# Kernel optimization log

Hardware: AMD Instinct MI355X
Metric: run time of the kernel (lower is better)

The kernel has to match this reference:

```python
import jax, jax.numpy as jnp
import numpy as np

N_WORD, N_TOPIC, N_DOC = 30000, 1000, 15000
D_WORD, D_TOPIC, D_OUT = 300, 300, 128
E = dict(ww=800000, wt=400000, wd=600000, td=300000, tt=150000)
SRC_N = dict(ww=N_WORD, wt=N_WORD, wd=N_WORD, td=N_TOPIC, tt=N_TOPIC)
DST_N = dict(ww=N_WORD, wt=N_TOPIC, wd=N_DOC, td=N_DOC, tt=N_TOPIC)


def setup_inputs() -> dict:
    key = jax.random.key(0)
    ks = iter(jax.random.split(key, 64))
    inp = {}
    inp["feat_word"] = jax.random.normal(next(ks), (N_WORD, D_WORD), jnp.float32)
    inp["feat_topic"] = jax.random.normal(next(ks), (N_TOPIC, D_TOPIC), jnp.float32)
    for et in ["ww", "wt", "wd", "td", "tt"]:
        inp[f"{et}_src"] = jax.random.randint(next(ks), (E[et],), 0, SRC_N[et], jnp.int32)
        inp[f"{et}_dst"] = jax.random.randint(next(ks), (E[et],), 0, DST_N[et], jnp.int32)
        inp[f"{et}_w"] = jax.random.uniform(next(ks), (E[et],), jnp.float32)
        din = D_WORD if et[0] == "w" else D_TOPIC
        inp[f"W_{et}"] = jax.random.normal(next(ks), (din, D_OUT), jnp.float32) / np.float32(np.sqrt(din))
        inp[f"b_{et}"] = jnp.zeros((D_OUT,), jnp.float32)
    return inp


def _mean_agg(Wh, src, dst, w, n_dst):
    # DGL fn.u_mul_e('Wh','weight','m') + fn.mean('m','h'): per-edge message
    # Wh[src] * w, mean-reduced per destination node (0 for isolated nodes).
    m = Wh[src] * w[:, None]                                   # [E, D_OUT]
    s = jax.ops.segment_sum(m, dst, num_segments=n_dst)        # [n_dst, D_OUT]
    c = jax.ops.segment_sum(jnp.ones_like(w), dst, num_segments=n_dst)
    return s / jnp.maximum(c, 1.0)[:, None]


def reference(feat_word, feat_topic,
              ww_src, ww_dst, ww_w, wt_src, wt_dst, wt_w,
              wd_src, wd_dst, wd_w, td_src, td_dst, td_w,
              tt_src, tt_dst, tt_w,
              W_ww, b_ww, W_wt, b_wt, W_wd, b_wd, W_td, b_td, W_tt, b_tt):
    # NOTE: the original forward's causal/noise branch is dead code --
    # `Wh = self.weight[etype](feat_dict[srctype])` overwrites it, so the
    # live math is a plain per-edge-type linear projection of source feats.
    Wh_ww = feat_word @ W_ww + b_ww
    Wh_wt = feat_word @ W_wt + b_wt
    Wh_wd = feat_word @ W_wd + b_wd
    Wh_td = feat_topic @ W_td + b_td
    Wh_tt = feat_topic @ W_tt + b_tt
    # multi_update_all(..., 'sum'): sum the per-etype means per dst node type.
    h_word = _mean_agg(Wh_ww, ww_src, ww_dst, ww_w, N_WORD)
    h_topic = (_mean_agg(Wh_wt, wt_src, wt_dst, wt_w, N_TOPIC)
               + _mean_agg(Wh_tt, tt_src, tt_dst, tt_w, N_TOPIC))
    h_doc = (_mean_agg(Wh_wd, wd_src, wd_dst, wd_w, N_DOC)
             + _mean_agg(Wh_td, td_src, td_dst, td_w, N_DOC))
    return (h_word, h_topic, h_doc)
```

## Files before the change

kernel.cpp:

```cpp
#include <hip/hip_runtime.h>

#define N_WORD 30000
#define N_TOPIC 1000
#define N_DOC 15000
#define DIN 300
#define KP 320
#define DOUT 128

#define E_WW 800000
#define E_WT 400000
#define E_WD 600000
#define E_TD 300000
#define E_TT 150000
#define E_TOTAL 2250000

#define CC_WW 0
#define CC_WT 30000
#define CC_WD 31000
#define CC_TD 46000
#define CC_TT 61000
#define NBINS 62000

#define CAP_WW 80
#define CAP_WT 544
#define CAP_WD 96
#define CAP_TD 56
#define CAP_TT 240
#define SB_WW 0
#define SB_WT (SB_WW + N_WORD * CAP_WW)
#define SB_WD (SB_WT + N_TOPIC * CAP_WT)
#define SB_TD (SB_WD + N_DOC * CAP_WD)
#define SB_TT (SB_TD + N_DOC * CAP_TD)
#define SLOT_TOTAL (SB_TT + N_TOPIC * CAP_TT)

#define NB_WW 59
#define NB_WT 32
#define NB_WD 30
#define NB_TD 30
#define NB_TT 32
#define CB_WW 0
#define CB_WT (CB_WW + 64 * NB_WW)
#define CB_WD (CB_WT + 64 * NB_WT)
#define CB_TD (CB_WD + 96 * NB_WD)
#define CB_TT (CB_TD + 48 * NB_TD)
#define COARSE_TOTAL (CB_TT + 24 * NB_TT)
#define NBK_TOTAL 183

#define CHUNK_BLOCKS 296
#define PREPW_BLOCKS 200

#define GW_BLOCKS 469
#define GT_BLOCKS 16
#define PKP 328

#define GB_TOPIC 250
#define GB_DOC 3750
#define GB_WORD 7500

using half8  = __attribute__((ext_vector_type(8))) _Float16;
using half2v = __attribute__((ext_vector_type(2))) _Float16;
using f32x4  = __attribute__((ext_vector_type(4))) float;

struct SegP {
    const int* src[5];
    const int* dst[5];
    const float* w[5];
};

struct WPtrs {
    const float* W[5];
    const float* b[5];
};

__device__ __forceinline__ void decode_chunk(
    int blk, int& ti, int& hx, int& ch, int& ne, int& nb, int& sh, int& cb)
{
    if (blk < 64)       { ti=0; hx=blk;     ch=12500; ne=E_WW; nb=NB_WW; sh=9; cb=CB_WW; }
    else if (blk < 128) { ti=1; hx=blk-64;  ch=6250;  ne=E_WT; nb=NB_WT; sh=5; cb=CB_WT; }
    else if (blk < 224) { ti=2; hx=blk-128; ch=6250;  ne=E_WD; nb=NB_WD; sh=9; cb=CB_WD; }
    else if (blk < 272) { ti=3; hx=blk-224; ch=6250;  ne=E_TD; nb=NB_TD; sh=9; cb=CB_TD; }
    else                { ti=4; hx=blk-272; ch=6250;  ne=E_TT; nb=NB_TT; sh=5; cb=CB_TT; }
}

__device__ __forceinline__ void decode_bucket(
    int g, int& b, int& nb, int& nblk, int& sh, int& N,
    int& cap, int& sb, int& cc, int& cb, int& bee)
{
    if (g < 59)       { b=g;     nb=NB_WW; nblk=64; sh=9; N=N_WORD;  cap=CAP_WW; sb=SB_WW; cc=CC_WW; cb=CB_WW; bee=800000; }
    else if (g < 91)  { b=g-59;  nb=NB_WT; nblk=64; sh=5; N=N_TOPIC; cap=CAP_WT; sb=SB_WT; cc=CC_WT; cb=CB_WT; bee=1200000; }
    else if (g < 121) { b=g-91;  nb=NB_WD; nblk=96; sh=9; N=N_DOC;   cap=CAP_WD; sb=SB_WD; cc=CC_WD; cb=CB_WD; bee=1800000; }
    else if (g < 151) { b=g-121; nb=NB_TD; nblk=48; sh=9; N=N_DOC;   cap=CAP_TD; sb=SB_TD; cc=CC_TD; cb=CB_TD; bee=2100000; }
    else              { b=g-151; nb=NB_TT; nblk=24; sh=5; N=N_TOPIC; cap=CAP_TT; sb=SB_TT; cc=CC_TT; cb=CB_TT; bee=2250000; }
}

__global__ __launch_bounds__(1024) void count_w(
    SegP S, int* __restrict__ coarse,
    WPtrs WP, _Float16* __restrict__ Wt_word, _Float16* __restrict__ Wt_topic,
    float* __restrict__ bcat_word, float* __restrict__ bcat_topic)
{
    __shared__ int hh[64];
    const int blk = blockIdx.x;
    if (blk < CHUNK_BLOCKS) {
        int ti, hx, ch, ne, nb, sh, cb;
        decode_chunk(blk, ti, hx, ch, ne, nb, sh, cb);
        if (threadIdx.x < 64) hh[threadIdx.x] = 0;
        __syncthreads();
        const int* __restrict__ dst = S.dst[ti];
        int lo = hx * ch;
        int hi = lo + ch; if (hi > ne) hi = ne;
        for (int i = lo + (int)threadIdx.x; i < hi; i += 1024)
            atomicAdd(&hh[dst[i] >> sh], 1);
        __syncthreads();
        if ((int)threadIdx.x < nb)
            coarse[cb + hx * nb + threadIdx.x] = hh[threadIdx.x];
    } else {
        int id = (blk - CHUNK_BLOCKS) * 1024 + (int)threadIdx.x;
        const int total = (384 + 256) * KP;
        if (id >= total) return;
        int ng = id / KP;
        int k = id - ng * KP;
        int mat, n, lng;
        _Float16* Wt;
        float* bc;
        if (ng < 384) { lng = ng; mat = lng >> 7; Wt = Wt_word; bc = bcat_word; }
        else          { lng = ng - 384; mat = 3 + (lng >> 7); Wt = Wt_topic; bc = bcat_topic; }
        n = lng & 127;
        Wt[(size_t)lng * KP + k] =
            (k < DIN) ? (_Float16)WP.W[mat][(size_t)k * DOUT + n] : (_Float16)0.f;
        if (k == 0) bc[lng] = WP.b[mat][n];
    }
}

template <int NJW>
__device__ __forceinline__ void gemm_cs(
    const float* __restrict__ A, int M,
    const _Float16* __restrict__ Wt, const float* __restrict__ bcat,
    _Float16* __restrict__ C, int Cstride, int rowBlk,
    _Float16* __restrict__ ldsA)
{
    const int t = threadIdx.x;
    const int lane = t & 63;
    const int w = t >> 6;
    const int lm = lane & 15;
    const int lq = lane >> 4;
    const int rowBase = rowBlk * 64;
    const int wc = w * (NJW * 16);

#pragma unroll
    for (int i = 0; i < 10; ++i) {
        int id = i * 256 + t;
        int row = id / 40;
        int c8 = id - row * 40;
        int k = c8 * 8;
        int grow = rowBase + row;
        half8 hv = half8{0, 0, 0, 0, 0, 0, 0, 0};
        if (grow < M) {
            const float* ap = A + (size_t)grow * DIN + k;
            if (k + 8 <= DIN) {
                float4 f0 = *(const float4*)ap;
                float4 f1 = *(const float4*)(ap + 4);
                hv = half8{(_Float16)f0.x, (_Float16)f0.y, (_Float16)f0.z,
                           (_Float16)f0.w, (_Float16)f1.x, (_Float16)f1.y,
                           (_Float16)f1.z, (_Float16)f1.w};
            } else if (k < DIN) {
#pragma unroll
                for (int j = 0; j < 8; ++j)
                    if (k + j < DIN) hv[j] = (_Float16)ap[j];
            }
        }
        *(half8*)&ldsA[row * PKP + k] = hv;
    }
    __syncthreads();

    f32x4 acc[4][NJW];
#pragma unroll
    for (int rt = 0; rt < 4; ++rt)
#pragma unroll
        for (int j = 0; j < NJW; ++j) acc[rt][j] = f32x4{0.f, 0.f, 0.f, 0.f};

#pragma unroll
    for (int s = 0; s < 10; ++s) {
        const int k0 = s * 32 + lq * 8;
        half8 bf[NJW];
#pragma unroll
        for (int j = 0; j < NJW; ++j)
            bf[j] = *(const half8*)&Wt[(size_t)(wc + j * 16 + lm) * KP + k0];
        half8 af[4];
#pragma unroll
        for (int rt = 0; rt < 4; ++rt)
            af[rt] = *(const half8*)&ldsA[(rt * 16 + lm) * PKP + k0];
#pragma unroll
        for (int rt = 0; rt < 4; ++rt)
#pragma unroll
            for (int j = 0; j < NJW; ++j)
                acc[rt][j] = __builtin_amdgcn_mfma_f32_16x16x32_f16(
                    af[rt], bf[j], acc[rt][j], 0, 0, 0);
    }

#pragma unroll
    for (int j = 0; j < NJW; ++j) {
        int col = wc + j * 16 + lm;
        float bias = bcat[col];
#pragma unroll
        for (int rt = 0; rt < 4; ++rt) {
#pragma unroll
            for (int reg = 0; reg < 4; ++reg) {
                int gr = rowBase + rt * 16 + lq * 4 + reg;
                if (gr < M)
                    C[(size_t)gr * Cstride + col] =
                        (_Float16)(acc[rt][j][reg] + bias);
            }
        }
    }
}

__global__ __launch_bounds__(256, 3) void pfx_gemm(
    int* __restrict__ coarse,
    const float* __restrict__ featw, const _Float16* __restrict__ Wtw,
    const float* __restrict__ bw, _Float16* __restrict__ Cw,
    const float* __restrict__ featt, const _Float16* __restrict__ Wtt,
    const float* __restrict__ bt, _Float16* __restrict__ Ct)
{
    __shared__ __align__(16) int usmem[10496];
    const int blk = blockIdx.x;
    if (blk == 0) {
        int* ttot = usmem;
        int* tpfx = usmem + 256;
        int g = threadIdx.x;
        int b, nb, nblk, sh, N, cap, sb, cc, cb, bee;
        if (g < NBK_TOTAL) {
            decode_bucket(g, b, nb, nblk, sh, N, cap, sb, cc, cb, bee);
            int tot = 0;
            for (int k = 0; k < nblk; ++k) tot += coarse[cb + k * nb + b];
            ttot[g] = tot;
        }
        __syncthreads();
        if (threadIdx.x == 0) {
            int run = 0;
            for (int i = 0; i < NBK_TOTAL; ++i) { tpfx[i] = run; run += ttot[i]; }
        }
        __syncthreads();
        if (g < NBK_TOTAL) {
            int run = tpfx[g];
            for (int k = 0; k < nblk; ++k) {
                int idx = cb + k * nb + b;
                int v = coarse[idx];
                coarse[idx] = run;
                run += v;
            }
        }
    } else if (blk < 1 + GW_BLOCKS) {
        gemm_cs<6>(featw, N_WORD, Wtw, bw, Cw, 384, blk - 1,
                   (_Float16*)usmem);
    } else {
        gemm_cs<4>(featt, N_TOPIC, Wtt, bt, Ct, 256, blk - 1 - GW_BLOCKS,
                   (_Float16*)usmem);
    }
}

__global__ __launch_bounds__(1024) void pass_a(
    SegP S, const int* __restrict__ coarse, int2* __restrict__ BE)
{
    __shared__ int cur[64];
    int ti, hx, ch, ne, nb, sh, cb;
    decode_chunk(blockIdx.x, ti, hx, ch, ne, nb, sh, cb);
    if ((int)threadIdx.x < nb)
        cur[threadIdx.x] = coarse[cb + hx * nb + threadIdx.x];
    __syncthreads();
    const int* __restrict__ dst = S.dst[ti];
    const int* __restrict__ src = S.src[ti];
    const float* __restrict__ wp = S.w[ti];
    int lo = hx * ch;
    int hi = lo + ch; if (hi > ne) hi = ne;
    for (int i = lo + (int)threadIdx.x; i < hi; i += 1024) {
        int d = dst[i];
        int p = atomicAdd(&cur[d >> sh], 1);
        unsigned short hw = __builtin_bit_cast(unsigned short, (_Float16)wp[i]);
        BE[p] = make_int2(d, src[i] | ((int)hw << 16));
    }
}

__global__ __launch_bounds__(1024) void pass_b(
    const int* __restrict__ coarse, const int2* __restrict__ BE,
    unsigned int* __restrict__ slots, int* __restrict__ cnt)
{
    __shared__ int cl[512];
    int b, nb, nblk, sh, N, cap, sb, cc, cb, bee;
    decode_bucket(blockIdx.x, b, nb, nblk, sh, N, cap, sb, cc, cb, bee);
    const int width = 1 << sh;
    const int n0 = b << sh;
    for (int j = threadIdx.x; j < width; j += 1024) cl[j] = 0;
    __syncthreads();
    int st = coarse[cb + b];
    int en = (b + 1 < nb) ? coarse[cb + b + 1] : bee;
    for (int i = st + (int)threadIdx.x; i < en; i += 1024) {
        int2 q = BE[i];
        int pos = atomicAdd(&cl[q.x - n0], 1);
        if (pos < cap)
            slots[(size_t)sb + (size_t)q.x * cap + pos] = (unsigned int)q.y;
    }
    __syncthreads();
    for (int j = threadIdx.x; j < width; j += 1024) {
        int d = n0 + j;
        if (d < N) cnt[cc + d] = cl[j];
    }
}

#define SV2(v, i) __builtin_shufflevector(v, v, i, i + 1)

__device__ __forceinline__ _Float16 wbits(unsigned int q)
{
    return __builtin_bit_cast(_Float16, (unsigned short)(q >> 16));
}

__device__ __forceinline__ void seg_mean16(
    const unsigned int* __restrict__ slots, int beg, int ce, int c,
    const _Float16* __restrict__ rowbase, int strideh, int ln, int sub,
    float a[8])
{
    half2v ac0 = half2v{0, 0}, ac1 = half2v{0, 0};
    half2v ac2 = half2v{0, 0}, ac3 = half2v{0, 0};
    int e = 0;
    for (; e + 16 <= ce; e += 16) {
        unsigned int q0 = slots[beg + e + 0 + sub];
        unsigned int q1 = slots[beg + e + 4 + sub];
        unsigned int q2 = slots[beg + e + 8 + sub];
        unsigned int q3 = slots[beg + e + 12 + sub];
        half8 v0 = *(const half8*)(rowbase + (size_t)(q0 & 0xFFFFu) * strideh + ln * 8);
        half8 v1 = *(const half8*)(rowbase + (size_t)(q1 & 0xFFFFu) * strideh + ln * 8);
        half8 v2 = *(const half8*)(rowbase + (size_t)(q2 & 0xFFFFu) * strideh + ln * 8);
        half8 v3 = *(const half8*)(rowbase + (size_t)(q3 & 0xFFFFu) * strideh + ln * 8);
        _Float16 h0 = wbits(q0), h1 = wbits(q1), h2 = wbits(q2), h3 = wbits(q3);
        half2v w0 = half2v{h0, h0}, w1 = half2v{h1, h1};
        half2v w2 = half2v{h2, h2}, w3 = half2v{h3, h3};
        ac0 += SV2(v0, 0) * w0 + SV2(v1, 0) * w1 + SV2(v2, 0) * w2 + SV2(v3, 0) * w3;
        ac1 += SV2(v0, 2) * w0 + SV2(v1, 2) * w1 + SV2(v2, 2) * w2 + SV2(v3, 2) * w3;
        ac2 += SV2(v0, 4) * w0 + SV2(v1, 4) * w1 + SV2(v2, 4) * w2 + SV2(v3, 4) * w3;
        ac3 += SV2(v0, 6) * w0 + SV2(v1, 6) * w1 + SV2(v2, 6) * w2 + SV2(v3, 6) * w3;
    }
    for (int e2 = e + sub; e2 < ce; e2 += 4) {
        unsigned int q = slots[beg + e2];
        half8 v = *(const half8*)(rowbase + (size_t)(q & 0xFFFFu) * strideh + ln * 8);
        _Float16 h = wbits(q);
        half2v wp = half2v{h, h};
        ac0 += SV2(v, 0) * wp;
        ac1 += SV2(v, 2) * wp;
        ac2 += SV2(v, 4) * wp;
        ac3 += SV2(v, 6) * wp;
    }
    a[0] = (float)ac0.x; a[1] = (float)ac0.y;
    a[2] = (float)ac1.x; a[3] = (float)ac1.y;
    a[4] = (float)ac2.x; a[5] = (float)ac2.y;
    a[6] = (float)ac3.x; a[7] = (float)ac3.y;
#pragma unroll
    for (int j = 0; j < 8; ++j) {
        a[j] += __shfl_down(a[j], 16);
        a[j] += __shfl_down(a[j], 32);
    }
    float inv = 1.0f / (float)(c > 1 ? c : 1);
#pragma unroll
    for (int j = 0; j < 8; ++j) a[j] *= inv;
}

__global__ __launch_bounds__(256) void gather_all(
    const unsigned int* __restrict__ slots, const int* __restrict__ cnt,
    const _Float16* __restrict__ Wh_word, const _Float16* __restrict__ Wh_topic,
    float* __restrict__ out_word, float* __restrict__ out_topic,
    float* __restrict__ out_doc)
{
    const int b = blockIdx.x;
    const int t = threadIdx.x;
    const int lane = t & 63;
    const int wv = t >> 6;
    const int sub = lane >> 4;
    const int ln = lane & 15;

    float a[8];
    float* outp;
    int node;

    if (b < GB_TOPIC) {
        node = b * 4 + wv;
        int c1 = cnt[CC_WT + node];
        int ce1 = c1 < CAP_WT ? c1 : CAP_WT;
        seg_mean16(slots, SB_WT + node * CAP_WT, ce1, c1, Wh_word + 128, 384, ln, sub, a);
        int c2 = cnt[CC_TT + node];
        int ce2 = c2 < CAP_TT ? c2 : CAP_TT;
        float a2[8];
        seg_mean16(slots, SB_TT + node * CAP_TT, ce2, c2, Wh_topic + 128, 256, ln, sub, a2);
#pragma unroll
        for (int j = 0; j < 8; ++j) a[j] += a2[j];
        outp = out_topic;
    } else if (b < GB_TOPIC + GB_DOC) {
        node = (b - GB_TOPIC) * 4 + wv;
        int c1 = cnt[CC_WD + node];
        int ce1 = c1 < CAP_WD ? c1 : CAP_WD;
        seg_mean16(slots, SB_WD + node * CAP_WD, ce1, c1, Wh_word + 256, 384, ln, sub, a);
        int c2 = cnt[CC_TD + node];
        int ce2 = c2 < CAP_TD ? c2 : CAP_TD;
        float a2[8];
        seg_mean16(slots, SB_TD + node * CAP_TD, ce2, c2, Wh_topic, 256, ln, sub, a2);
#pragma unroll
        for (int j = 0; j < 8; ++j) a[j] += a2[j];
        outp = out_doc;
    } else {
        node = (b - GB_TOPIC - GB_DOC) * 4 + wv;
        int c = cnt[CC_WW + node];
        int ce = c < CAP_WW ? c : CAP_WW;
        seg_mean16(slots, SB_WW + node * CAP_WW, ce, c, Wh_word, 384, ln, sub, a);
        outp = out_word;
    }

    if (sub == 0) {
        float4* o = (float4*)outp + (size_t)node * 32 + ln * 2;
        o[0] = make_float4(a[0], a[1], a[2], a[3]);
        o[1] = make_float4(a[4], a[5], a[6], a[7]);
    }
}

extern "C" void kernel_launch(void* const* d_in, const int* in_sizes, int n_in,
                              void* d_out, int out_size, void* d_ws, size_t ws_size,
                              hipStream_t stream)
{
    const float* feat_word  = (const float*)d_in[0];
    const float* feat_topic = (const float*)d_in[1];

    const int*   ww_src = (const int*)d_in[2];
    const int*   ww_dst = (const int*)d_in[3];
    const float* ww_w   = (const float*)d_in[4];
    const float* W_ww   = (const float*)d_in[5];
    const float* b_ww   = (const float*)d_in[6];

    const int*   wt_src = (const int*)d_in[7];
    const int*   wt_dst = (const int*)d_in[8];
    const float* wt_w   = (const float*)d_in[9];
    const float* W_wt   = (const float*)d_in[10];
    const float* b_wt   = (const float*)d_in[11];

    const int*   wd_src = (const int*)d_in[12];
    const int*   wd_dst = (const int*)d_in[13];
    const float* wd_w   = (const float*)d_in[14];
    const float* W_wd   = (const float*)d_in[15];
    const float* b_wd   = (const float*)d_in[16];

    const int*   td_src = (const int*)d_in[17];
    const int*   td_dst = (const int*)d_in[18];
    const float* td_w   = (const float*)d_in[19];
    const float* W_td   = (const float*)d_in[20];
    const float* b_td   = (const float*)d_in[21];

    const int*   tt_src = (const int*)d_in[22];
    const int*   tt_dst = (const int*)d_in[23];
    const float* tt_w   = (const float*)d_in[24];
    const float* W_tt   = (const float*)d_in[25];
    const float* b_tt   = (const float*)d_in[26];

    char* wsb = (char*)d_ws;
    size_t off = 0;
    _Float16* Wh_word  = (_Float16*)(wsb + off); off += (size_t)N_WORD * 384 * 2;
    _Float16* Wh_topic = (_Float16*)(wsb + off); off += (size_t)N_TOPIC * 256 * 2;
    _Float16* Wt_word  = (_Float16*)(wsb + off); off += (size_t)384 * KP * 2;
    _Float16* Wt_topic = (_Float16*)(wsb + off); off += (size_t)256 * KP * 2;
    float* bcat_word   = (float*)(wsb + off);    off += 384 * 4;
    float* bcat_topic  = (float*)(wsb + off);    off += 256 * 4;
    unsigned int* slots = (unsigned int*)(wsb + off); off += (size_t)SLOT_TOTAL * 4;
    int* cnt_all       = (int*)(wsb + off);      off += (size_t)NBINS * 4;
    int* coarse        = (int*)(wsb + off);      off += (size_t)COARSE_TOTAL * 4;
    int2* BE           = (int2*)(wsb + off);     off += (size_t)E_TOTAL * 8;

    float* out_word  = (float*)d_out;
    float* out_topic = out_word + (size_t)N_WORD * DOUT;
    float* out_doc   = out_topic + (size_t)N_TOPIC * DOUT;

    SegP S;
    S.src[0] = ww_src; S.dst[0] = ww_dst; S.w[0] = ww_w;
    S.src[1] = wt_src; S.dst[1] = wt_dst; S.w[1] = wt_w;
    S.src[2] = wd_src; S.dst[2] = wd_dst; S.w[2] = wd_w;
    S.src[3] = td_src; S.dst[3] = td_dst; S.w[3] = td_w;
    S.src[4] = tt_src; S.dst[4] = tt_dst; S.w[4] = tt_w;

    WPtrs WP;
    WP.W[0] = W_ww; WP.W[1] = W_wt; WP.W[2] = W_wd; WP.W[3] = W_td; WP.W[4] = W_tt;
    WP.b[0] = b_ww; WP.b[1] = b_wt; WP.b[2] = b_wd; WP.b[3] = b_td; WP.b[4] = b_tt;

    count_w<<<CHUNK_BLOCKS + PREPW_BLOCKS, 1024, 0, stream>>>(
        S, coarse, WP, Wt_word, Wt_topic, bcat_word, bcat_topic);
    pfx_gemm<<<1 + GW_BLOCKS + GT_BLOCKS, 256, 0, stream>>>(
        coarse,
        feat_word, Wt_word, bcat_word, Wh_word,
        feat_topic, Wt_topic, bcat_topic, Wh_topic);
    pass_a<<<CHUNK_BLOCKS, 1024, 0, stream>>>(S, coarse, BE);
    pass_b<<<NBK_TOTAL, 1024, 0, stream>>>(coarse, BE, slots, cnt_all);
    gather_all<<<GB_TOPIC + GB_DOC + GB_WORD, 256, 0, stream>>>(
        slots, cnt_all, Wh_word, Wh_topic, out_word, out_topic, out_doc);

    (void)in_sizes; (void)n_in; (void)ws_size;
}
```

Measured before the change: 301.0 us.

## Privatize per-wave LDS histograms, stage GEMM epilogue through LDS, batch prefix loads

The count and scatter passes now keep one LDS histogram per wavefront instead of one per block, which cuts contention on shared-memory atomics. pass_a recounts its chunk so it can give each wave its own offset range. The GEMM epilogue writes results into LDS and then stores coalesced 16-byte rows instead of scattered 2-byte stores. The prefix scan loads counts eight at a time. The costs are an extra read of dst in pass_a and extra barriers in the epilogue, and there is also an odd no-op bias-pointer assignment.

```diff
diff --git a/kernel.cpp b/kernel.cpp
--- a/kernel.cpp
+++ b/kernel.cpp
@@ -98,21 +98,27 @@
     WPtrs WP, _Float16* __restrict__ Wt_word, _Float16* __restrict__ Wt_topic,
     float* __restrict__ bcat_word, float* __restrict__ bcat_topic)
 {
-    __shared__ int hh[64];
+    __shared__ int wcnt[16][64];
     const int blk = blockIdx.x;
     if (blk < CHUNK_BLOCKS) {
         int ti, hx, ch, ne, nb, sh, cb;
         decode_chunk(blk, ti, hx, ch, ne, nb, sh, cb);
-        if (threadIdx.x < 64) hh[threadIdx.x] = 0;
+        const int w = threadIdx.x >> 6;
+        const int lane = threadIdx.x & 63;
+        wcnt[w][lane] = 0;
         __syncthreads();
         const int* __restrict__ dst = S.dst[ti];
         int lo = hx * ch;
         int hi = lo + ch; if (hi > ne) hi = ne;
         for (int i = lo + (int)threadIdx.x; i < hi; i += 1024)
-            atomicAdd(&hh[dst[i] >> sh], 1);
+            atomicAdd(&wcnt[w][dst[i] >> sh], 1);
         __syncthreads();
-        if ((int)threadIdx.x < nb)
-            coarse[cb + hx * nb + threadIdx.x] = hh[threadIdx.x];
+        if ((int)threadIdx.x < nb) {
+            int s = 0;
+#pragma unroll
+            for (int k = 0; k < 16; ++k) s += wcnt[k][threadIdx.x];
+            coarse[cb + hx * nb + threadIdx.x] = s;
+        }
     } else {
         int id = (blk - CHUNK_BLOCKS) * 1024 + (int)threadIdx.x;
         const int total = (384 + 256) * KP;
@@ -197,19 +203,34 @@
                     af[rt], bf[j], acc[rt][j], 0, 0, 0);
     }
 
-#pragma unroll
-    for (int j = 0; j < NJW; ++j) {
-        int col = wc + j * 16 + lm;
-        float bias = bcat[col];
-#pragma unroll
-        for (int rt = 0; rt < 4; ++rt) {
-#pragma unroll
-            for (int reg = 0; reg < 4; ++reg) {
-                int gr = rowBase + rt * 16 + lq * 4 + reg;
-                if (gr < M)
-                    C[(size_t)gr * Cstride + col] =
-                        (_Float16)(acc[rt][j][reg] + bias);
+    const int HCOLS = NJW * 32;
+    const int HPAD = HCOLS + 8;
+    const int nch = HCOLS / 8;
+#pragma unroll
+    for (int h = 0; h < 2; ++h) {
+        __syncthreads();
+        if ((w >> 1) == h) {
+            int wl = w & 1;
+#pragma unroll
+            for (int j = 0; j < NJW; ++j) {
+                int lc = wl * (NJW * 16) + j * 16 + lm;
+                float bias = bcat[h * HCOLS + lc];
+#pragma unroll
+                for (int rt = 0; rt < 4; ++rt)
+#pragma unroll
+                    for (int reg = 0; reg < 4; ++reg)
+                        ldsA[(rt * 16 + lq * 4 + reg) * HPAD + lc] =
+                            (_Float16)(acc[rt][j][reg] + bias);
             }
+        }
+        __syncthreads();
+        for (int id = t; id < 64 * nch; id += 256) {
+            int row = id / nch;
+            int c8 = id - row * nch;
+            int gr = rowBase + row;
+            if (gr < M)
+                *(half8*)&C[(size_t)gr * Cstride + h * HCOLS + c8 * 8] =
+                    *(const half8*)&ldsA[row * HPAD + c8 * 8];
         }
     }
 }
@@ -231,7 +252,13 @@
         if (g < NBK_TOTAL) {
             decode_bucket(g, b, nb, nblk, sh, N, cap, sb, cc, cb, bee);
             int tot = 0;
-            for (int k = 0; k < nblk; ++k) tot += coarse[cb + k * nb + b];
+            for (int k0 = 0; k0 < nblk; k0 += 8) {
+                int v[8];
+#pragma unroll
+                for (int j = 0; j < 8; ++j) v[j] = coarse[cb + (k0 + j) * nb + b];
+#pragma unroll
+                for (int j = 0; j < 8; ++j) tot += v[j];
+            }
             ttot[g] = tot;
         }
         __syncthreads();
@@ -242,11 +269,15 @@
         __syncthreads();
         if (g < NBK_TOTAL) {
             int run = tpfx[g];
-            for (int k = 0; k < nblk; ++k) {
-                int idx = cb + k * nb + b;
-                int v = coarse[idx];
-                coarse[idx] = run;
-                run += v;
+            for (int k0 = 0; k0 < nblk; k0 += 8) {
+                int v[8];
+#pragma unroll
+                for (int j = 0; j < 8; ++j) v[j] = coarse[cb + (k0 + j) * nb + b];
+#pragma unroll
+                for (int j = 0; j < 8; ++j) {
+                    coarse[cb + (k0 + j) * nb + b] = run;
+                    run += v[j];
+                }
             }
         }
     } else if (blk < 1 + GW_BLOCKS) {
@@ -261,20 +292,34 @@
 __global__ __launch_bounds__(1024) void pass_a(
     SegP S, const int* __restrict__ coarse, int2* __restrict__ BE)
 {
-    __shared__ int cur[64];
+    __shared__ int wcnt[16][64];
     int ti, hx, ch, ne, nb, sh, cb;
     decode_chunk(blockIdx.x, ti, hx, ch, ne, nb, sh, cb);
-    if ((int)threadIdx.x < nb)
-        cur[threadIdx.x] = coarse[cb + hx * nb + threadIdx.x];
+    const int w = threadIdx.x >> 6;
+    const int lane = threadIdx.x & 63;
+    wcnt[w][lane] = 0;
     __syncthreads();
     const int* __restrict__ dst = S.dst[ti];
     const int* __restrict__ src = S.src[ti];
     const float* __restrict__ wp = S.w[ti];
     int lo = hx * ch;
     int hi = lo + ch; if (hi > ne) hi = ne;
+    for (int i = lo + (int)threadIdx.x; i < hi; i += 1024)
+        atomicAdd(&wcnt[w][dst[i] >> sh], 1);
+    __syncthreads();
+    if ((int)threadIdx.x < nb) {
+        int run = coarse[cb + hx * nb + threadIdx.x];
+#pragma unroll
+        for (int k = 0; k < 16; ++k) {
+            int v = wcnt[k][threadIdx.x];
+            wcnt[k][threadIdx.x] = run;
+            run += v;
+        }
+    }
+    __syncthreads();
     for (int i = lo + (int)threadIdx.x; i < hi; i += 1024) {
         int d = dst[i];
-        int p = atomicAdd(&cur[d >> sh], 1);
+        int p = atomicAdd(&wcnt[w][d >> sh], 1);
         unsigned short hw = __builtin_bit_cast(unsigned short, (_Float16)wp[i]);
         BE[p] = make_int2(d, src[i] | ((int)hw << 16));
     }
@@ -481,7 +526,7 @@
 
     WPtrs WP;
     WP.W[0] = W_ww; WP.W[1] = W_wt; WP.W[2] = W_wd; WP.W[3] = W_td; WP.W[4] = W_tt;
-    WP.b[0] = b_ww; WP.b[1] = b_wt; WP.b[2] = b_wd; WP.b[3] = b_td; WP.b[4] = b_tt;
+    WP.b[0] = b_ww; WP.b[1] = b_wt; WP.b[2] = b_wd; WP.b[3] = b_tt ? W_tt == W_tt ? b_tt : b_td : b_td; WP.b[3] = b_td; WP.b[4] = b_tt;
 
     count_w<<<CHUNK_BLOCKS + PREPW_BLOCKS, 1024, 0, stream>>>(
         S, coarse, WP, Wt_word, Wt_topic, bcat_word, bcat_topic);
```

Result: faster. 292.4 us (-2.9%).
